# Kernel tuning notes

Hardware: AMD Instinct MI355X
Metric: run time of the kernel (lower is better)

## Reference

```python
import jax, jax.numpy as jnp
import numpy as np

N_NODES = 100000
N_EDGES = 800000
HIDDEN = 128


def setup_inputs() -> dict:
    key = jax.random.key(0)
    ks = jax.random.split(key, 9)
    h_n = jax.random.normal(ks[0], (N_NODES, HIDDEN), dtype=jnp.float32)
    edge_src = jax.random.randint(ks[1], (N_EDGES,), 0, N_NODES, dtype=jnp.int32)
    edge_dst = jax.random.randint(ks[2], (N_EDGES,), 0, N_NODES, dtype=jnp.int32)
    s = 0.05
    W_w = jax.random.normal(ks[3], (HIDDEN, HIDDEN), dtype=jnp.float32) * s
    W_b = jax.random.normal(ks[4], (HIDDEN,), dtype=jnp.float32) * s
    Ws_w = jax.random.normal(ks[5], (HIDDEN, HIDDEN), dtype=jnp.float32) * s
    Ws_b = jax.random.normal(ks[6], (HIDDEN,), dtype=jnp.float32) * s
    Wt_w = jax.random.normal(ks[7], (HIDDEN, HIDDEN), dtype=jnp.float32) * s
    Wt_b = jax.random.normal(ks[8], (HIDDEN,), dtype=jnp.float32) * s
    return {"h_n": h_n, "edge_src": edge_src, "edge_dst": edge_dst,
            "W_w": W_w, "W_b": W_b, "Ws_w": Ws_w, "Ws_b": Ws_b,
            "Wt_w": Wt_w, "Wt_b": Wt_b}


def reference(h_n, edge_src, edge_dst, W_w, W_b, Ws_w, Ws_b, Wt_w, Wt_b):
    # Dense linears (nn.Linear: x @ W.T + b)
    Wh = h_n @ W_w.T + W_b        # [N,H] used for A @ W(h)
    Wsh = h_n @ Ws_w.T + Ws_b     # [N,H] self term
    Wth = h_n @ Wt_w.T + Wt_b     # [N,H] used for A.T @ W_trans(h)
    # A[src,dst] = 1:  (A @ X)[i]   = sum over edges (i,j) of X[j]
    #              (A.T @ X)[j] = sum over edges (i,j) of X[i]
    agg_fwd = jax.ops.segment_sum(Wh[edge_dst], edge_src, num_segments=N_NODES)
    agg_bwd = jax.ops.segment_sum(Wth[edge_src], edge_dst, num_segments=N_NODES)
    return jax.nn.relu(agg_fwd + Wsh + agg_bwd)
```

## Files before the change

### kernel.cpp

```cpp
#include <hip/hip_runtime.h>
#include <hip/hip_bf16.h>

#define NN 100000
#define NE 800000
#define HIDDEN 128
#define NED (2 * NE)
#define BKN 64
#define NBF 1563
#define BCAP 2048
#define PS 7
#define CHUNK 8192
#define PBLK ((NED + CHUNK - 1) / CHUNK)

typedef __attribute__((ext_vector_type(8))) short bf16x8;
typedef __attribute__((ext_vector_type(4))) short bf16x4;
typedef __attribute__((ext_vector_type(4))) float f32x4;

__device__ __forceinline__ short f2bf(float f) {
  union { float f; unsigned u; } x; x.f = f;
  unsigned r = x.u + 0x7fffu + ((x.u >> 16) & 1u);
  return (short)(r >> 16);
}
__device__ __forceinline__ float bf2f(short s) {
  union { unsigned u; float f; } x;
  x.u = ((unsigned)(unsigned short)s) << 16;
  return x.f;
}

__global__ __launch_bounds__(256) void convert_all(
    const float* __restrict__ h, const float* __restrict__ m0,
    const float* __restrict__ m1, const float* __restrict__ m2,
    short* __restrict__ h_bf, short* __restrict__ Wbf) {
  int blk = blockIdx.x;
  int tid = threadIdx.x;
  if (blk < 12500) {
    int i = blk * 256 + tid;
    f32x4 v = *(const f32x4*)(h + (size_t)i * 4);
    bf16x4 o;
#pragma unroll
    for (int j = 0; j < 4; j++) o[j] = f2bf(v[j]);
    *(bf16x4*)(h_bf + (size_t)i * 4) = o;
  } else {
    int i = (blk - 12500) * 256 + tid;
    int m = i >> 14, j = i & 16383;
    const float* s = (m == 0) ? m0 : (m == 1) ? m1 : m2;
    Wbf[i] = f2bf(s[j]);
  }
}

__global__ __launch_bounds__(256) void edge_scatter(
    const int* __restrict__ esrc, const int* __restrict__ edst,
    int* __restrict__ gcur, unsigned* __restrict__ ELP) {
  __shared__ int lcur[NBF];
  __shared__ int loff[NBF];
  __shared__ int gbase[NBF];
  __shared__ int psum[256];
  __shared__ unsigned buf[CHUNK];
  __shared__ unsigned short bidA[CHUNK];
  int tid = threadIdx.x;
  for (int i = tid; i < NBF; i += 256) lcur[i] = 0;
  __syncthreads();
  int base = blockIdx.x * CHUNK;
  int nit = min(CHUNK, NED - base);
  for (int k = tid; k < nit; k += 256) {
    int ed = base + k;
    int b = (ed < NE) ? (esrc[ed] >> 6) : (edst[ed - NE] >> 6);
    atomicAdd(&lcur[b], 1);
  }
  __syncthreads();
  int s = 0;
  int lo0 = tid * PS, hi0 = min(NBF, tid * PS + PS);
  for (int j = lo0; j < hi0; j++) s += lcur[j];
  psum[tid] = s;
  __syncthreads();
  for (int off = 1; off < 256; off <<= 1) {
    int x = psum[tid];
    int add = (tid >= off) ? psum[tid - off] : 0;
    __syncthreads();
    psum[tid] = x + add;
    __syncthreads();
  }
  int run = psum[tid] - s;
  for (int j = lo0; j < hi0; j++) { loff[j] = run; run += lcur[j]; }
  __syncthreads();
  for (int b = tid; b < NBF; b += 256) {
    int c = lcur[b];
    if (c) gbase[b] = atomicAdd(gcur + b, c);
    lcur[b] = loff[b];
  }
  __syncthreads();
  for (int k = tid; k < nit; k += 256) {
    int ed = base + k;
    int b, tl, nbr, dir;
    if (ed < NE) { int tg = esrc[ed]; nbr = edst[ed]; b = tg >> 6; tl = tg & 63; dir = 0; }
    else { int e2 = ed - NE; int tg = edst[e2]; nbr = esrc[e2]; b = tg >> 6; tl = tg & 63; dir = 1; }
    int slot = atomicAdd(&lcur[b], 1);
    buf[slot] = ((unsigned)dir << 23) | ((unsigned)tl << 17) | (unsigned)nbr;
    bidA[slot] = (unsigned short)b;
  }
  __syncthreads();
  for (int i = tid; i < nit; i += 256) {
    int b = bidA[i];
    int dst = gbase[b] + (i - loff[b]);
    if (dst < BCAP) ELP[(size_t)b * BCAP + dst] = buf[i];
  }
}

#define ACC8(V) { a0f+=bf2f((V)[0]); a1f+=bf2f((V)[1]); a2f+=bf2f((V)[2]); a3f+=bf2f((V)[3]); \
                  a4f+=bf2f((V)[4]); a5f+=bf2f((V)[5]); a6f+=bf2f((V)[6]); a7f+=bf2f((V)[7]); }
#define MACC8(M,V) { a0f=fmaf(M,bf2f((V)[0]),a0f); a1f=fmaf(M,bf2f((V)[1]),a1f); \
                     a2f=fmaf(M,bf2f((V)[2]),a2f); a3f=fmaf(M,bf2f((V)[3]),a3f); \
                     a4f=fmaf(M,bf2f((V)[4]),a4f); a5f=fmaf(M,bf2f((V)[5]),a5f); \
                     a6f=fmaf(M,bf2f((V)[6]),a6f); a7f=fmaf(M,bf2f((V)[7]),a7f); }
__global__ __launch_bounds__(512, 4) void fused_gather_gemm(
    const short* __restrict__ h_bf, const unsigned* __restrict__ ELP,
    const int* __restrict__ gcur, const short* __restrict__ Wbf,
    const float* __restrict__ Wb, const float* __restrict__ Wsb,
    const float* __restrict__ Wtb, float* __restrict__ out) {
  __shared__ int sorted[BCAP];
  __shared__ int cnt[128];
  __shared__ int pfx[128];
  __shared__ int cur[128];
  __shared__ short Ht[64 * 128];
  __shared__ short At2[2 * 64 * 128];
  int tid = threadIdx.x;
  int blk = blockIdx.x;
  int node0 = blk * BKN;
  const unsigned* elp = ELP + (size_t)blk * BCAP;
  int n = min(gcur[blk], BCAP);
  if (tid < 128) cnt[tid] = 0;
  __syncthreads();
  for (int k = tid; k < n; k += 512) atomicAdd(&cnt[elp[k] >> 17], 1);
  for (int p = tid; p < 1024; p += 512) {
    int row = p >> 4, c = p & 15;
    int nd = node0 + row;
    bf16x8 hv = {0, 0, 0, 0, 0, 0, 0, 0};
    if (nd < NN) hv = *(const bf16x8*)(h_bf + (size_t)nd * HIDDEN + c * 8);
    *(bf16x8*)(Ht + row * 128 + ((c ^ (row & 7)) * 8)) = hv;
  }
  __syncthreads();
  int v = (tid < 128) ? cnt[tid] : 0;
  if (tid < 128) pfx[tid] = v;
  __syncthreads();
  for (int off = 1; off < 128; off <<= 1) {
    int add = (tid < 128 && tid >= off) ? pfx[tid - off] : 0;
    __syncthreads();
    if (tid < 128) pfx[tid] += add;
    __syncthreads();
  }
  if (tid < 128) cur[tid] = pfx[tid] - cnt[tid];
  __syncthreads();
  for (int k = tid; k < n; k += 512) {
    unsigned pv = elp[k];
    int slot = atomicAdd(&cur[pv >> 17], 1);
    sorted[slot] = (int)(pv & 0x1FFFFu);
  }
  __syncthreads();
  int qw = tid >> 4, q = tid & 15;
  const short* hb = h_bf + (size_t)q * 8;
#pragma unroll
  for (int t = 0; t < 4; t++) {
    int nd = qw * 4 + t;
    int b0 = pfx[nd];
    int deg = cnt[nd];
    int a0 = b0 - deg;
    float a0f = 0.f, a1f = 0.f, a2f = 0.f, a3f = 0.f;
    float a4f = 0.f, a5f = 0.f, a6f = 0.f, a7f = 0.f;
    if (deg > 0) {
      int lastp = b0 - 1;
      int i0 = sorted[a0];
      int i1 = sorted[min(a0 + 1, lastp)];
      int i2 = sorted[min(a0 + 2, lastp)];
      int i3 = sorted[min(a0 + 3, lastp)];
      bf16x8 v0 = *(const bf16x8*)(hb + (size_t)i0 * HIDDEN);
      bf16x8 v1 = *(const bf16x8*)(hb + (size_t)i1 * HIDDEN);
      bf16x8 v2 = *(const bf16x8*)(hb + (size_t)i2 * HIDDEN);
      bf16x8 v3 = *(const bf16x8*)(hb + (size_t)i3 * HIDDEN);
      int j = a0;
      int ni0 = sorted[min(j + 4, lastp)];
      int ni1 = sorted[min(j + 5, lastp)];
      int ni2 = sorted[min(j + 6, lastp)];
      int ni3 = sorted[min(j + 7, lastp)];
      while (j + 4 <= b0) {
        ACC8(v0); v0 = *(const bf16x8*)(hb + (size_t)ni0 * HIDDEN);
        ACC8(v1); v1 = *(const bf16x8*)(hb + (size_t)ni1 * HIDDEN);
        ACC8(v2); v2 = *(const bf16x8*)(hb + (size_t)ni2 * HIDDEN);
        ACC8(v3); v3 = *(const bf16x8*)(hb + (size_t)ni3 * HIDDEN);
        j += 4;
        ni0 = sorted[min(j + 4, lastp)];
        ni1 = sorted[min(j + 5, lastp)];
        ni2 = sorted[min(j + 6, lastp)];
        ni3 = sorted[min(j + 7, lastp)];
      }
      int r = b0 - j;
      float m1 = (r > 0) ? 1.f : 0.f;
      float m2 = (r > 1) ? 1.f : 0.f;
      float m3 = (r > 2) ? 1.f : 0.f;
      MACC8(m1, v0); MACC8(m2, v1); MACC8(m3, v2);
    }
    short* dst = At2 + (nd >> 6) * 8192 + (nd & 63) * 128 + ((q ^ (nd & 7)) * 8);
    bf16x8 o;
    o[0] = f2bf(a0f); o[1] = f2bf(a1f); o[2] = f2bf(a2f); o[3] = f2bf(a3f);
    o[4] = f2bf(a4f); o[5] = f2bf(a5f); o[6] = f2bf(a6f); o[7] = f2bf(a7f);
    *(bf16x8*)dst = o;
  }
  __syncthreads();
  int lane = tid & 63;
  int m16 = lane & 15;
  int kq  = lane >> 4;
  int col0 = (tid >> 6) * 16;
  int key = m16 & 7;
  bf16x8 wf[3][4];
#pragma unroll
  for (int i = 0; i < 3; i++)
#pragma unroll
    for (int t = 0; t < 4; t++)
      wf[i][t] = *(const bf16x8*)(Wbf + i * 16384 + (col0 + m16) * 128 + t * 32 + kq * 8);
  f32x4 bW = *(const f32x4*)(Wb  + col0 + kq * 4);
  f32x4 bS = *(const f32x4*)(Wsb + col0 + kq * 4);
  f32x4 bT = *(const f32x4*)(Wtb + col0 + kq * 4);
#pragma unroll
  for (int g = 0; g < 4; g++) {
    f32x4 acc = {0.f, 0.f, 0.f, 0.f};
    int rl = g * 16 + m16;
    const short* hrow = Ht  + rl * 128;
    const short* arow = At2 + rl * 128;
#pragma unroll
    for (int t = 0; t < 4; t++) {
      int pc = (kq + 4 * t) ^ key;
      bf16x8 a0v = *(const bf16x8*)(hrow + pc * 8);
      acc = __builtin_amdgcn_mfma_f32_16x16x32_bf16(wf[0][t], a0v, acc, 0, 0, 0);
    }
#pragma unroll
    for (int i = 1; i < 3; i++)
#pragma unroll
      for (int t = 0; t < 4; t++) {
        int pc = (kq + 4 * t) ^ key;
        bf16x8 af = *(const bf16x8*)(arow + (i - 1) * 8192 + pc * 8);
        acc = __builtin_amdgcn_mfma_f32_16x16x32_bf16(wf[i][t], af, acc, 0, 0, 0);
      }
    int r = node0 + rl;
    if (r < NN) {
      float dF = (float)cnt[rl];
      float dB = (float)cnt[64 + rl];
      f32x4 vv;
#pragma unroll
      for (int j = 0; j < 4; j++)
        vv[j] = fmaxf(acc[j] + bS[j] + dF * bW[j] + dB * bT[j], 0.f);
      *(f32x4*)(out + (size_t)r * HIDDEN + col0 + kq * 4) = vv;
    }
  }
}

extern "C" void kernel_launch(void* const* d_in, const int* in_sizes, int n_in,
                              void* d_out, int out_size, void* d_ws, size_t ws_size,
                              hipStream_t stream) {
  const float* h    = (const float*)d_in[0];
  const int*   esrc = (const int*)d_in[1];
  const int*   edst = (const int*)d_in[2];
  const float* Ww   = (const float*)d_in[3];
  const float* Wb   = (const float*)d_in[4];
  const float* Wsw  = (const float*)d_in[5];
  const float* Wsb  = (const float*)d_in[6];
  const float* Wtw  = (const float*)d_in[7];
  const float* Wtb  = (const float*)d_in[8];
  float* out = (float*)d_out;

  char* ws = (char*)d_ws;
  int*      gcur = (int*)(ws + 0);
  unsigned* ELP  = (unsigned*)(ws + 6400);
  short*    Wbf  = (short*)(ws + 12810496);
  short*    h_bf = (short*)(ws + 12908800);

  hipMemsetAsync(gcur, 0, NBF * sizeof(int), stream);

  convert_all<<<12692, 256, 0, stream>>>(h, Wsw, Ww, Wtw, h_bf, Wbf);
  edge_scatter<<<PBLK, 256, 0, stream>>>(esrc, edst, gcur, ELP);
  fused_gather_gemm<<<NBF, 512, 0, stream>>>(
      h_bf, ELP, gcur, Wbf, Wb, Wsb, Wtb, out);
}
```

Baseline: 249.9 us.

## Split gather into two halves reusing one LDS tile to raise occupancy

The fused gather+GEMM kernel now aggregates forward and backward neighbour sums in two separate passes that share a single 64x128 bf16 LDS buffer. Each pass is followed by the matching MFMA work, with accumulators held across passes. Launch bounds move from 4 to 6 blocks per CU. The aim is to cut LDS use and weight-fragment register pressure so more blocks stay resident and hide gather latency. The cost is two extra barriers and less parallel gather work per phase.

```diff
diff --git a/kernel.cpp b/kernel.cpp
--- a/kernel.cpp
+++ b/kernel.cpp
@@ -106,13 +106,7 @@
   }
 }
 
-#define ACC8(V) { a0f+=bf2f((V)[0]); a1f+=bf2f((V)[1]); a2f+=bf2f((V)[2]); a3f+=bf2f((V)[3]); \
-                  a4f+=bf2f((V)[4]); a5f+=bf2f((V)[5]); a6f+=bf2f((V)[6]); a7f+=bf2f((V)[7]); }
-#define MACC8(M,V) { a0f=fmaf(M,bf2f((V)[0]),a0f); a1f=fmaf(M,bf2f((V)[1]),a1f); \
-                     a2f=fmaf(M,bf2f((V)[2]),a2f); a3f=fmaf(M,bf2f((V)[3]),a3f); \
-                     a4f=fmaf(M,bf2f((V)[4]),a4f); a5f=fmaf(M,bf2f((V)[5]),a5f); \
-                     a6f=fmaf(M,bf2f((V)[6]),a6f); a7f=fmaf(M,bf2f((V)[7]),a7f); }
-__global__ __launch_bounds__(512, 4) void fused_gather_gemm(
+__global__ __launch_bounds__(512, 6) void fused_gather_gemm(
     const short* __restrict__ h_bf, const unsigned* __restrict__ ELP,
     const int* __restrict__ gcur, const short* __restrict__ Wbf,
     const float* __restrict__ Wb, const float* __restrict__ Wsb,
@@ -122,7 +116,7 @@
   __shared__ int pfx[128];
   __shared__ int cur[128];
   __shared__ short Ht[64 * 128];
-  __shared__ short At2[2 * 64 * 128];
+  __shared__ short At[64 * 128];
   int tid = threadIdx.x;
   int blk = blockIdx.x;
   int node0 = blk * BKN;
@@ -156,98 +150,147 @@
     sorted[slot] = (int)(pv & 0x1FFFFu);
   }
   __syncthreads();
+
   int qw = tid >> 4, q = tid & 15;
   const short* hb = h_bf + (size_t)q * 8;
-#pragma unroll
-  for (int t = 0; t < 4; t++) {
-    int nd = qw * 4 + t;
-    int b0 = pfx[nd];
-    int deg = cnt[nd];
-    int a0 = b0 - deg;
-    float a0f = 0.f, a1f = 0.f, a2f = 0.f, a3f = 0.f;
-    float a4f = 0.f, a5f = 0.f, a6f = 0.f, a7f = 0.f;
-    if (deg > 0) {
-      int lastp = b0 - 1;
-      int i0 = sorted[a0];
-      int i1 = sorted[min(a0 + 1, lastp)];
-      int i2 = sorted[min(a0 + 2, lastp)];
-      int i3 = sorted[min(a0 + 3, lastp)];
-      bf16x8 v0 = *(const bf16x8*)(hb + (size_t)i0 * HIDDEN);
-      bf16x8 v1 = *(const bf16x8*)(hb + (size_t)i1 * HIDDEN);
-      bf16x8 v2 = *(const bf16x8*)(hb + (size_t)i2 * HIDDEN);
-      bf16x8 v3 = *(const bf16x8*)(hb + (size_t)i3 * HIDDEN);
-      int j = a0;
-      int ni0 = sorted[min(j + 4, lastp)];
-      int ni1 = sorted[min(j + 5, lastp)];
-      int ni2 = sorted[min(j + 6, lastp)];
-      int ni3 = sorted[min(j + 7, lastp)];
-      while (j + 4 <= b0) {
-        ACC8(v0); v0 = *(const bf16x8*)(hb + (size_t)ni0 * HIDDEN);
-        ACC8(v1); v1 = *(const bf16x8*)(hb + (size_t)ni1 * HIDDEN);
-        ACC8(v2); v2 = *(const bf16x8*)(hb + (size_t)ni2 * HIDDEN);
-        ACC8(v3); v3 = *(const bf16x8*)(hb + (size_t)ni3 * HIDDEN);
-        j += 4;
-        ni0 = sorted[min(j + 4, lastp)];
-        ni1 = sorted[min(j + 5, lastp)];
-        ni2 = sorted[min(j + 6, lastp)];
-        ni3 = sorted[min(j + 7, lastp)];
-      }
-      int r = b0 - j;
-      float m1 = (r > 0) ? 1.f : 0.f;
-      float m2 = (r > 1) ? 1.f : 0.f;
-      float m3 = (r > 2) ? 1.f : 0.f;
-      MACC8(m1, v0); MACC8(m2, v1); MACC8(m3, v2);
-    }
-    short* dst = At2 + (nd >> 6) * 8192 + (nd & 63) * 128 + ((q ^ (nd & 7)) * 8);
-    bf16x8 o;
-    o[0] = f2bf(a0f); o[1] = f2bf(a1f); o[2] = f2bf(a2f); o[3] = f2bf(a3f);
-    o[4] = f2bf(a4f); o[5] = f2bf(a5f); o[6] = f2bf(a6f); o[7] = f2bf(a7f);
-    *(bf16x8*)dst = o;
-  }
-  __syncthreads();
   int lane = tid & 63;
   int m16 = lane & 15;
   int kq  = lane >> 4;
   int col0 = (tid >> 6) * 16;
   int key = m16 & 7;
-  bf16x8 wf[3][4];
-#pragma unroll
-  for (int i = 0; i < 3; i++)
-#pragma unroll
-    for (int t = 0; t < 4; t++)
-      wf[i][t] = *(const bf16x8*)(Wbf + i * 16384 + (col0 + m16) * 128 + t * 32 + kq * 8);
-  f32x4 bW = *(const f32x4*)(Wb  + col0 + kq * 4);
-  f32x4 bS = *(const f32x4*)(Wsb + col0 + kq * 4);
-  f32x4 bT = *(const f32x4*)(Wtb + col0 + kq * 4);
-#pragma unroll
-  for (int g = 0; g < 4; g++) {
-    f32x4 acc = {0.f, 0.f, 0.f, 0.f};
-    int rl = g * 16 + m16;
-    const short* hrow = Ht  + rl * 128;
-    const short* arow = At2 + rl * 128;
+  f32x4 acc[4];
+#pragma unroll
+  for (int g = 0; g < 4; g++) acc[g] = (f32x4){0.f, 0.f, 0.f, 0.f};
+
+  auto gather_half = [&](int vbase) {
+#pragma unroll
+    for (int t = 0; t < 2; t++) {
+      int nd = vbase + qw * 2 + t;
+      int b0 = pfx[nd];
+      int deg = cnt[nd];
+      int a0 = b0 - deg;
+      float a0f = 0.f, a1f = 0.f, a2f = 0.f, a3f = 0.f;
+      float a4f = 0.f, a5f = 0.f, a6f = 0.f, a7f = 0.f;
+      if (deg > 0) {
+        int lastp = b0 - 1;
+        int i0 = sorted[a0];
+        int i1 = sorted[min(a0 + 1, lastp)];
+        int i2 = sorted[min(a0 + 2, lastp)];
+        int i3 = sorted[min(a0 + 3, lastp)];
+        bf16x8 v0 = *(const bf16x8*)(hb + (size_t)i0 * HIDDEN);
+        bf16x8 v1 = *(const bf16x8*)(hb + (size_t)i1 * HIDDEN);
+        bf16x8 v2 = *(const bf16x8*)(hb + (size_t)i2 * HIDDEN);
+        bf16x8 v3 = *(const bf16x8*)(hb + (size_t)i3 * HIDDEN);
+        int j = a0;
+        int ni0 = sorted[min(j + 4, lastp)];
+        int ni1 = sorted[min(j + 5, lastp)];
+        int ni2 = sorted[min(j + 6, lastp)];
+        int ni3 = sorted[min(j + 7, lastp)];
+        while (j + 4 <= b0) {
+          float w0 = bf2f(v0[0]);
+          a0f += bf2f(v0[0]); a1f += bf2f(v0[1]); a2f += bf2f(v0[2]); a3f += bf2f(v0[3]);
+          a4f += bf2f(v0[4]); a5f += bf2f(v0[5]); a6f += bf2f(v0[6]); a7f += bf2f(v0[7]);
+          v0 = *(const bf16x8*)(hb + (size_t)ni0 * HIDDEN);
+          a0f += bf2f(v1[0]); a1f += bf2f(v1[1]); a2f += bf2f(v1[2]); a3f += bf2f(v1[3]);
+          a4f += bf2f(v1[4]); a5f += bf2f(v1[5]); a6f += bf2f(v1[6]); a7f += bf2f(v1[7]);
+          v1 = *(const bf16x8*)(hb + (size_t)ni1 * HIDDEN);
+          a0f += bf2f(v2[0]); a1f += bf2f(v2[1]); a2f += bf2f(v2[2]); a3f += bf2f(v2[3]);
+          a4f += bf2f(v2[4]); a5f += bf2f(v2[5]); a6f += bf2f(v2[6]); a7f += bf2f(v2[7]);
+          v2 = *(const bf16x8*)(hb + (size_t)ni2 * HIDDEN);
+          a0f += bf2f(v3[0]); a1f += bf2f(v3[1]); a2f += bf2f(v3[2]); a3f += bf2f(v3[3]);
+          a4f += bf2f(v3[4]); a5f += bf2f(v3[5]); a6f += bf2f(v3[6]); a7f += bf2f(v3[7]);
+          v3 = *(const bf16x8*)(hb + (size_t)ni3 * HIDDEN);
+          j += 4;
+          ni0 = sorted[min(j + 4, lastp)];
+          ni1 = sorted[min(j + 5, lastp)];
+          ni2 = sorted[min(j + 6, lastp)];
+          ni3 = sorted[min(j + 7, lastp)];
+          (void)w0;
+        }
+        int r = b0 - j;
+        float m1 = (r > 0) ? 1.f : 0.f;
+        float m2 = (r > 1) ? 1.f : 0.f;
+        float m3 = (r > 2) ? 1.f : 0.f;
+        a0f = fmaf(m1, bf2f(v0[0]), a0f); a1f = fmaf(m1, bf2f(v0[1]), a1f);
+        a2f = fmaf(m1, bf2f(v0[2]), a2f); a3f = fmaf(m1, bf2f(v0[3]), a3f);
+        a4f = fmaf(m1, bf2f(v0[4]), a4f); a5f = fmaf(m1, bf2f(v0[5]), a5f);
+        a6f = fmaf(m1, bf2f(v0[6]), a6f); a7f = fmaf(m1, bf2f(v0[7]), a7f);
+        a0f = fmaf(m2, bf2f(v1[0]), a0f); a1f = fmaf(m2, bf2f(v1[1]), a1f);
+        a2f = fmaf(m2, bf2f(v1[2]), a2f); a3f = fmaf(m2, bf2f(v1[3]), a3f);
+        a4f = fmaf(m2, bf2f(v1[4]), a4f); a5f = fmaf(m2, bf2f(v1[5]), a5f);
+        a6f = fmaf(m2, bf2f(v1[6]), a6f); a7f = fmaf(m2, bf2f(v1[7]), a7f);
+        a0f = fmaf(m3, bf2f(v2[0]), a0f); a1f = fmaf(m3, bf2f(v2[1]), a1f);
+        a2f = fmaf(m3, bf2f(v2[2]), a2f); a3f = fmaf(m3, bf2f(v2[3]), a3f);
+        a4f = fmaf(m3, bf2f(v2[4]), a4f); a5f = fmaf(m3, bf2f(v2[5]), a5f);
+        a6f = fmaf(m3, bf2f(v2[6]), a6f); a7f = fmaf(m3, bf2f(v2[7]), a7f);
+      }
+      short* dst = At + (nd & 63) * 128 + ((q ^ (nd & 7)) * 8);
+      bf16x8 o;
+      o[0] = f2bf(a0f); o[1] = f2bf(a1f); o[2] = f2bf(a2f); o[3] = f2bf(a3f);
+      o[4] = f2bf(a4f); o[5] = f2bf(a5f); o[6] = f2bf(a6f); o[7] = f2bf(a7f);
+      *(bf16x8*)dst = o;
+    }
+  };
+
+  gather_half(0);
+  __syncthreads();
+  {
+    bf16x8 wfS[4], wfF[4];
 #pragma unroll
     for (int t = 0; t < 4; t++) {
-      int pc = (kq + 4 * t) ^ key;
-      bf16x8 a0v = *(const bf16x8*)(hrow + pc * 8);
-      acc = __builtin_amdgcn_mfma_f32_16x16x32_bf16(wf[0][t], a0v, acc, 0, 0, 0);
+      wfS[t] = *(const bf16x8*)(Wbf + 0 * 16384 + (col0 + m16) * 128 + t * 32 + kq * 8);
+      wfF[t] = *(const bf16x8*)(Wbf + 1 * 16384 + (col0 + m16) * 128 + t * 32 + kq * 8);
     }
 #pragma unroll
-    for (int i = 1; i < 3; i++)
+    for (int g = 0; g < 4; g++) {
+      int rl = g * 16 + m16;
+      const short* hrow = Ht + rl * 128;
+      const short* arow = At + rl * 128;
 #pragma unroll
       for (int t = 0; t < 4; t++) {
         int pc = (kq + 4 * t) ^ key;
-        bf16x8 af = *(const bf16x8*)(arow + (i - 1) * 8192 + pc * 8);
-        acc = __builtin_amdgcn_mfma_f32_16x16x32_bf16(wf[i][t], af, acc, 0, 0, 0);
-      }
-    int r = node0 + rl;
-    if (r < NN) {
-      float dF = (float)cnt[rl];
-      float dB = (float)cnt[64 + rl];
-      f32x4 vv;
-#pragma unroll
-      for (int j = 0; j < 4; j++)
-        vv[j] = fmaxf(acc[j] + bS[j] + dF * bW[j] + dB * bT[j], 0.f);
-      *(f32x4*)(out + (size_t)r * HIDDEN + col0 + kq * 4) = vv;
+        bf16x8 hv = *(const bf16x8*)(hrow + pc * 8);
+        acc[g] = __builtin_amdgcn_mfma_f32_16x16x32_bf16(wfS[t], hv, acc[g], 0, 0, 0);
+      }
+#pragma unroll
+      for (int t = 0; t < 4; t++) {
+        int pc = (kq + 4 * t) ^ key;
+        bf16x8 av = *(const bf16x8*)(arow + pc * 8);
+        acc[g] = __builtin_amdgcn_mfma_f32_16x16x32_bf16(wfF[t], av, acc[g], 0, 0, 0);
+      }
+    }
+  }
+  __syncthreads();
+  gather_half(64);
+  __syncthreads();
+  {
+    bf16x8 wfT[4];
+#pragma unroll
+    for (int t = 0; t < 4; t++)
+      wfT[t] = *(const bf16x8*)(Wbf + 2 * 16384 + (col0 + m16) * 128 + t * 32 + kq * 8);
+    f32x4 bW = *(const f32x4*)(Wb  + col0 + kq * 4);
+    f32x4 bS = *(const f32x4*)(Wsb + col0 + kq * 4);
+    f32x4 bT = *(const f32x4*)(Wtb + col0 + kq * 4);
+#pragma unroll
+    for (int g = 0; g < 4; g++) {
+      int rl = g * 16 + m16;
+      const short* arow = At + rl * 128;
+#pragma unroll
+      for (int t = 0; t < 4; t++) {
+        int pc = (kq + 4 * t) ^ key;
+        bf16x8 av = *(const bf16x8*)(arow + pc * 8);
+        acc[g] = __builtin_amdgcn_mfma_f32_16x16x32_bf16(wfT[t], av, acc[g], 0, 0, 0);
+      }
+      int r = node0 + rl;
+      if (r < NN) {
+        float dF = (float)cnt[rl];
+        float dB = (float)cnt[64 + rl];
+        f32x4 vv;
+#pragma unroll
+        for (int j = 0; j < 4; j++)
+          vv[j] = fmaxf(acc[g][j] + bS[j] + dF * bW[j] + dB * bT[j], 0.f);
+        *(f32x4*)(out + (size_t)r * HIDDEN + col0 + kq * 4) = vv;
+      }
     }
   }
 }
```

Result: no change. 245.8 us, median of 2 (-1.6%).

## Split gather into two halves sharing one LDS aggregate buffer to raise occupancy

Applied to the files above, without the earlier changes.

The gathered forward and backward aggregates are now produced one half at a time into a single 64x128 LDS buffer instead of a double-sized one. Each half is consumed by its MFMA pass before the next half is gathered, and four accumulators persist across both passes. This shrinks LDS and weight-register footprint, and launch bounds rise from 4 to 6 blocks per CU. The cost is extra barriers and less memory-level parallelism per thread, since each thread now gathers two nodes per phase instead of four.

```diff
diff --git a/kernel.cpp b/kernel.cpp
--- a/kernel.cpp
+++ b/kernel.cpp
@@ -112,7 +112,89 @@
                      a2f=fmaf(M,bf2f((V)[2]),a2f); a3f=fmaf(M,bf2f((V)[3]),a3f); \
                      a4f=fmaf(M,bf2f((V)[4]),a4f); a5f=fmaf(M,bf2f((V)[5]),a5f); \
                      a6f=fmaf(M,bf2f((V)[6]),a6f); a7f=fmaf(M,bf2f((V)[7]),a7f); }
-__global__ __launch_bounds__(512, 4) void fused_gather_gemm(
+#define GATHER_HALF(VBASE) \
+  _Pragma("unroll") \
+  for (int t = 0; t < 2; t++) { \
+    int nd = (VBASE) + qw * 2 + t; \
+    int b0 = pfx[nd]; \
+    int deg = cnt[nd]; \
+    int a0 = b0 - deg; \
+    float a0f = 0.f, a1f = 0.f, a2f = 0.f, a3f = 0.f; \
+    float a4f = 0.f, a5f = 0.f, a6f = 0.f, a7f = 0.f; \
+    if (deg > 0) { \
+      int lastp = b0 - 1; \
+      int i0 = sorted[a0]; \
+      int i1 = sorted[min(a0 + 1, lastp)]; \
+      int i2 = sorted[min(a0 + 2, lastp)]; \
+      int i3 = sorted[min(a0 + 3, lastp)]; \
+      bf16x8 v0 = *(const bf16x8*)(hb + (size_t)i0 * HIDDEN); \
+      bf16x8 v1 = *(const bf16x8*)(hb + (size_t)i1 * HIDDEN); \
+      bf16x8 v2 = *(const bf16x8*)(hb + (size_t)i2 * HIDDEN); \
+      bf16x8 v3 = *(const bf16x8*)(hb + (size_t)i3 * HIDDEN); \
+      int j = a0; \
+      int ni0 = sorted[min(j + 4, lastp)]; \
+      int ni1 = sorted[min(j + 5, lastp)]; \
+      int ni2 = sorted[min(j + 6, lastp)]; \
+      int ni3 = sorted[min(j + 7, lastp)]; \
+      while (j + 4 <= b0) { \
+        ACC8(v0); v0 = *(const bf16x8*)(hb + (size_t)ni0 * HIDDEN); \
+        ACC8(v1); v1 = *(const bf16x8*)(hb + (size_t)ni1 * HIDDEN); \
+        ACC8(v2); v2 = *(const bf16x8*)(hb + (size_t)ni2 * HIDDEN); \
+        ACC8(v3); v3 = *(const bf16x8*)(hb + (size_t)ni3 * HIDDEN); \
+        j += 4; \
+        ni0 = sorted[min(j + 4, lastp)]; \
+        ni1 = sorted[min(j + 5, lastp)]; \
+        ni2 = sorted[min(j + 6, lastp)]; \
+        ni3 = sorted[min(j + 7, lastp)]; \
+      } \
+      int rrem = b0 - j; \
+      float m1 = (rrem > 0) ? 1.f : 0.f; \
+      float m2 = (rrem > 1) ? 1.f : 0.f; \
+      float m3 = (rrem > 2) ? 1.f : 0.f; \
+      MACC8(m1, v0); MACC8(m2, v1); MACC8(m3, v2); \
+    } \
+    short* dst = At + (nd & 63) * 128 + ((q ^ (nd & 7)) * 8); \
+    bf16x8 o; \
+    o[0] = f2bf(a0f); o[1] = f2bf(a1f); o[2] = f2bf(a2f); o[3] = f2bf(a3f); \
+    o[4] = f2bf(a4f); o[5] = f2bf(a5f); o[6] = f2bf(a6f); o[7] = f2bf(a7f); \
+    *(bf16x8*)dst = o; \
+  }
+#define C1_STEP(G, ACCV) { \
+  int rl = (G) * 16 + m16; \
+  const short* hrow = Ht + rl * 128; \
+  const short* arow = At + rl * 128; \
+  _Pragma("unroll") \
+  for (int t = 0; t < 4; t++) { \
+    int pc = (kq + 4 * t) ^ key; \
+    bf16x8 hv = *(const bf16x8*)(hrow + pc * 8); \
+    ACCV = __builtin_amdgcn_mfma_f32_16x16x32_bf16(wfS[t], hv, ACCV, 0, 0, 0); \
+  } \
+  _Pragma("unroll") \
+  for (int t = 0; t < 4; t++) { \
+    int pc = (kq + 4 * t) ^ key; \
+    bf16x8 av = *(const bf16x8*)(arow + pc * 8); \
+    ACCV = __builtin_amdgcn_mfma_f32_16x16x32_bf16(wfF[t], av, ACCV, 0, 0, 0); \
+  } }
+#define C2_STEP(G, ACCV) { \
+  int rl = (G) * 16 + m16; \
+  const short* arow = At + rl * 128; \
+  _Pragma("unroll") \
+  for (int t = 0; t < 4; t++) { \
+    int pc = (kq + 4 * t) ^ key; \
+    bf16x8 av = *(const bf16x8*)(arow + pc * 8); \
+    ACCV = __builtin_amdgcn_mfma_f32_16x16x32_bf16(wfT[t], av, ACCV, 0, 0, 0); \
+  } \
+  int r = node0 + rl; \
+  if (r < NN) { \
+    float dF = (float)cnt[rl]; \
+    float dB = (float)cnt[64 + rl]; \
+    f32x4 vv; \
+    _Pragma("unroll") \
+    for (int jj = 0; jj < 4; jj++) \
+      vv[jj] = fmaxf(ACCV[jj] + bS[jj] + dF * bW[jj] + dB * bT[jj], 0.f); \
+    *(f32x4*)(out + (size_t)r * HIDDEN + col0 + kq * 4) = vv; \
+  } }
+__global__ __launch_bounds__(512, 6) void fused_gather_gemm(
     const short* __restrict__ h_bf, const unsigned* __restrict__ ELP,
     const int* __restrict__ gcur, const short* __restrict__ Wbf,
     const float* __restrict__ Wb, const float* __restrict__ Wsb,
@@ -122,7 +204,7 @@
   __shared__ int pfx[128];
   __shared__ int cur[128];
   __shared__ short Ht[64 * 128];
-  __shared__ short At2[2 * 64 * 128];
+  __shared__ short At[64 * 128];
   int tid = threadIdx.x;
   int blk = blockIdx.x;
   int node0 = blk * BKN;
@@ -156,99 +238,48 @@
     sorted[slot] = (int)(pv & 0x1FFFFu);
   }
   __syncthreads();
+
   int qw = tid >> 4, q = tid & 15;
   const short* hb = h_bf + (size_t)q * 8;
-#pragma unroll
-  for (int t = 0; t < 4; t++) {
-    int nd = qw * 4 + t;
-    int b0 = pfx[nd];
-    int deg = cnt[nd];
-    int a0 = b0 - deg;
-    float a0f = 0.f, a1f = 0.f, a2f = 0.f, a3f = 0.f;
-    float a4f = 0.f, a5f = 0.f, a6f = 0.f, a7f = 0.f;
-    if (deg > 0) {
-      int lastp = b0 - 1;
-      int i0 = sorted[a0];
-      int i1 = sorted[min(a0 + 1, lastp)];
-      int i2 = sorted[min(a0 + 2, lastp)];
-      int i3 = sorted[min(a0 + 3, lastp)];
-      bf16x8 v0 = *(const bf16x8*)(hb + (size_t)i0 * HIDDEN);
-      bf16x8 v1 = *(const bf16x8*)(hb + (size_t)i1 * HIDDEN);
-      bf16x8 v2 = *(const bf16x8*)(hb + (size_t)i2 * HIDDEN);
-      bf16x8 v3 = *(const bf16x8*)(hb + (size_t)i3 * HIDDEN);
-      int j = a0;
-      int ni0 = sorted[min(j + 4, lastp)];
-      int ni1 = sorted[min(j + 5, lastp)];
-      int ni2 = sorted[min(j + 6, lastp)];
-      int ni3 = sorted[min(j + 7, lastp)];
-      while (j + 4 <= b0) {
-        ACC8(v0); v0 = *(const bf16x8*)(hb + (size_t)ni0 * HIDDEN);
-        ACC8(v1); v1 = *(const bf16x8*)(hb + (size_t)ni1 * HIDDEN);
-        ACC8(v2); v2 = *(const bf16x8*)(hb + (size_t)ni2 * HIDDEN);
-        ACC8(v3); v3 = *(const bf16x8*)(hb + (size_t)ni3 * HIDDEN);
-        j += 4;
-        ni0 = sorted[min(j + 4, lastp)];
-        ni1 = sorted[min(j + 5, lastp)];
-        ni2 = sorted[min(j + 6, lastp)];
-        ni3 = sorted[min(j + 7, lastp)];
-      }
-      int r = b0 - j;
-      float m1 = (r > 0) ? 1.f : 0.f;
-      float m2 = (r > 1) ? 1.f : 0.f;
-      float m3 = (r > 2) ? 1.f : 0.f;
-      MACC8(m1, v0); MACC8(m2, v1); MACC8(m3, v2);
-    }
-    short* dst = At2 + (nd >> 6) * 8192 + (nd & 63) * 128 + ((q ^ (nd & 7)) * 8);
-    bf16x8 o;
-    o[0] = f2bf(a0f); o[1] = f2bf(a1f); o[2] = f2bf(a2f); o[3] = f2bf(a3f);
-    o[4] = f2bf(a4f); o[5] = f2bf(a5f); o[6] = f2bf(a6f); o[7] = f2bf(a7f);
-    *(bf16x8*)dst = o;
-  }
-  __syncthreads();
   int lane = tid & 63;
   int m16 = lane & 15;
   int kq  = lane >> 4;
   int col0 = (tid >> 6) * 16;
   int key = m16 & 7;
-  bf16x8 wf[3][4];
+  f32x4 acc0 = {0.f, 0.f, 0.f, 0.f};
+  f32x4 acc1 = {0.f, 0.f, 0.f, 0.f};
+  f32x4 acc2 = {0.f, 0.f, 0.f, 0.f};
+  f32x4 acc3 = {0.f, 0.f, 0.f, 0.f};
+
+  GATHER_HALF(0)
+  __syncthreads();
+  {
+    bf16x8 wfS[4], wfF[4];
 #pragma unroll
-  for (int i = 0; i < 3; i++)
+    for (int t = 0; t < 4; t++) {
+      wfS[t] = *(const bf16x8*)(Wbf + 0 * 16384 + (col0 + m16) * 128 + t * 32 + kq * 8);
+      wfF[t] = *(const bf16x8*)(Wbf + 1 * 16384 + (col0 + m16) * 128 + t * 32 + kq * 8);
+    }
+    C1_STEP(0, acc0)
+    C1_STEP(1, acc1)
+    C1_STEP(2, acc2)
+    C1_STEP(3, acc3)
+  }
+  __syncthreads();
+  GATHER_HALF(64)
+  __syncthreads();
+  {
+    bf16x8 wfT[4];
 #pragma unroll
     for (int t = 0; t < 4; t++)
-      wf[i][t] = *(const bf16x8*)(Wbf + i * 16384 + (col0 + m16) * 128 + t * 32 + kq * 8);
-  f32x4 bW = *(const f32x4*)(Wb  + col0 + kq * 4);
-  f32x4 bS = *(const f32x4*)(Wsb + col0 + kq * 4);
-  f32x4 bT = *(const f32x4*)(Wtb + col0 + kq * 4);
-#pragma unroll
-  for (int g = 0; g < 4; g++) {
-    f32x4 acc = {0.f, 0.f, 0.f, 0.f};
-    int rl = g * 16 + m16;
-    const short* hrow = Ht  + rl * 128;
-    const short* arow = At2 + rl * 128;
-#pragma unroll
-    for (int t = 0; t < 4; t++) {
-      int pc = (kq + 4 * t) ^ key;
-      bf16x8 a0v = *(const bf16x8*)(hrow + pc * 8);
-      acc = __builtin_amdgcn_mfma_f32_16x16x32_bf16(wf[0][t], a0v, acc, 0, 0, 0);
-    }
-#pragma unroll
-    for (int i = 1; i < 3; i++)
-#pragma unroll
-      for (int t = 0; t < 4; t++) {
-        int pc = (kq + 4 * t) ^ key;
-        bf16x8 af = *(const bf16x8*)(arow + (i - 1) * 8192 + pc * 8);
-        acc = __builtin_amdgcn_mfma_f32_16x16x32_bf16(wf[i][t], af, acc, 0, 0, 0);
-      }
-    int r = node0 + rl;
-    if (r < NN) {
-      float dF = (float)cnt[rl];
-      float dB = (float)cnt[64 + rl];
-      f32x4 vv;
-#pragma unroll
-      for (int j = 0; j < 4; j++)
-        vv[j] = fmaxf(acc[j] + bS[j] + dF * bW[j] + dB * bT[j], 0.f);
-      *(f32x4*)(out + (size_t)r * HIDDEN + col0 + kq * 4) = vv;
-    }
+      wfT[t] = *(const bf16x8*)(Wbf + 2 * 16384 + (col0 + m16) * 128 + t * 32 + kq * 8);
+    f32x4 bW = *(const f32x4*)(Wb  + col0 + kq * 4);
+    f32x4 bS = *(const f32x4*)(Wsb + col0 + kq * 4);
+    f32x4 bT = *(const f32x4*)(Wtb + col0 + kq * 4);
+    C2_STEP(0, acc0)
+    C2_STEP(1, acc1)
+    C2_STEP(2, acc2)
+    C2_STEP(3, acc3)
   }
 }
 
```

After: 255.1 us. +2.1%, slower.
